# Performance work log

Measured on AMD Instinct MI355X. Metric: run time of the kernel, lower is better.

## Reference

```python
import jax, jax.numpy as jnp
import numpy as np

# DeepSeek-V2-Lite MoE dims
E = 64      # n_routed_experts
H = 2048    # hidden_size
I = 1408    # moe_intermediate_size
K = 6       # num_experts_per_tok (top-k)
T = 1024    # tokens
C = 256     # per-expert capacity (expected load T*K/E = 96; 256 is ample, no drops with seed 0)


def setup_inputs() -> dict:
    key = jax.random.key(0)
    k1, k2, k3, k4 = jax.random.split(key, 4)
    return {
        "hidden_states": jax.random.normal(k1, (T, H), jnp.float32),
        "gate_w": jax.random.normal(k2, (H, E), jnp.float32) * 0.02,   # LiteLinear(H->E), no bias
        "w1": jax.random.normal(k3, (E, H, I), jnp.float32) * 0.02,    # experts_w1
        "w2": jax.random.normal(k4, (E, I, H), jnp.float32) * 0.02,    # experts_w2
    }


def _moe(x, gate_w, w1, w2):
    # Router: softmax gate + top-k + renormalize (vLLM fused_moe renormalize=True)
    logits = x @ gate_w                                    # [T, E]
    probs = jax.nn.softmax(logits, axis=-1)
    topk_w, topk_idx = jax.lax.top_k(probs, K)             # [T, K]
    topk_w = topk_w / jnp.sum(topk_w, axis=-1, keepdims=True)

    # Dispatch: flatten (token, k) pairs, compute slot position within each expert
    P = T * K
    e_p = topk_idx.reshape(P)                              # expert id per pair
    onehot = (e_p[:, None] == jnp.arange(E)[None, :]).astype(jnp.int32)  # [P, E]
    pos = jnp.cumsum(onehot, axis=0) - 1                   # running count per expert
    pos = jnp.take_along_axis(pos, e_p[:, None], axis=1)[:, 0]           # [P]
    valid = pos < C
    pos_c = jnp.where(valid, pos, 0)
    fvalid = valid[:, None].astype(x.dtype)

    x_pair = jnp.repeat(x, K, axis=0)                      # [P, H]
    xe = jnp.zeros((E, C, H), x.dtype).at[e_p, pos_c].add(x_pair * fvalid)  # [E, C, H]

    # Grouped expert GEMMs: silu(x @ w1) @ w2
    h = jax.nn.silu(jnp.einsum('ech,ehi->eci', xe, w1))    # [E, C, I]
    ye = jnp.einsum('eci,eih->ech', h, w2)                 # [E, C, H]

    # Combine: gather back per pair, weight by routing prob, sum over k
    y_pair = ye[e_p, pos_c] * fvalid                       # [P, H]
    out = (y_pair.reshape(T, K, H) * topk_w[..., None]).sum(axis=1)
    return out


def reference(hidden_states, gate_w, w1, w2):
    return _moe(hidden_states, gate_w, w1, w2)
```

## Files before the change

### kernel.cpp

```cpp
#include <hip/hip_runtime.h>

#define T_TOK 1024
#define H_DIM 2048
#define I_DIM 1408
#define E_NUM 64
#define K_TOP 6
#define CAP   256
#define P_NUM (T_TOK * K_TOP)

typedef __bf16 bf16x8 __attribute__((ext_vector_type(8)));
typedef float  f32x4  __attribute__((ext_vector_type(4)));
typedef unsigned int uint32x2 __attribute__((ext_vector_type(2)));
typedef unsigned int uint32x4 __attribute__((ext_vector_type(4)));

__device__ inline unsigned pack2bf16(float a, float b) {
    unsigned short au = __builtin_bit_cast(unsigned short, (__bf16)a);
    unsigned short bu = __builtin_bit_cast(unsigned short, (__bf16)b);
    return (unsigned)au | ((unsigned)bu << 16);
}

__device__ inline void wg_barrier() {
    __builtin_amdgcn_sched_barrier(0);
    asm volatile("s_waitcnt lgkmcnt(0)");
    __builtin_amdgcn_s_barrier();
    __builtin_amdgcn_sched_barrier(0);
}

__global__ __launch_bounds__(256) void router_kernel(
        const float* __restrict__ x, const float* __restrict__ gw,
        float* __restrict__ tw, int* __restrict__ ti, __bf16* __restrict__ xb,
        float* __restrict__ out)
{
    const int t0  = blockIdx.x * 4;
    const int tid = threadIdx.x;
    __shared__ float xs[4][H_DIM];
    __shared__ float part[4][4][E_NUM];

    {
        f32x4 z = (f32x4){0.f, 0.f, 0.f, 0.f};
        f32x4* ob = (f32x4*)(out + (size_t)t0 * H_DIM);
        #pragma unroll
        for (int i = 0; i < 8; ++i) ob[i * 256 + tid] = z;
    }

    #pragma unroll
    for (int tt = 0; tt < 4; ++tt) {
        #pragma unroll
        for (int i = 0; i < 8; ++i) {
            float v = x[(size_t)(t0 + tt) * H_DIM + i * 256 + tid];
            xs[tt][i * 256 + tid] = v;
            xb[(size_t)(t0 + tt) * H_DIM + i * 256 + tid] = (__bf16)v;
        }
    }
    __syncthreads();

    const int e = tid & 63, q = tid >> 6;
    float a0 = 0.f, a1 = 0.f, a2 = 0.f, a3 = 0.f;
    for (int hh = q * 512; hh < q * 512 + 512; ++hh) {
        float g = gw[hh * E_NUM + e];
        a0 += xs[0][hh] * g; a1 += xs[1][hh] * g;
        a2 += xs[2][hh] * g; a3 += xs[3][hh] * g;
    }
    part[q][0][e] = a0; part[q][1][e] = a1; part[q][2][e] = a2; part[q][3][e] = a3;
    __syncthreads();

    const int tt = q;
    float l = part[0][tt][e] + part[1][tt][e] + part[2][tt][e] + part[3][tt][e];
    float m = l;
    #pragma unroll
    for (int s = 32; s; s >>= 1) m = fmaxf(m, __shfl_xor(m, s));
    float p = __expf(l - m);
    float sum = p;
    #pragma unroll
    for (int s = 32; s; s >>= 1) sum += __shfl_xor(sum, s);
    float prob = p / sum;

    float v = prob, wsum = 0.f;
    float tv[K_TOP]; int tix[K_TOP];
    #pragma unroll
    for (int k = 0; k < K_TOP; ++k) {
        float bv = v; int bi = e;
        #pragma unroll
        for (int s = 32; s; s >>= 1) {
            float ov = __shfl_xor(bv, s); int oi = __shfl_xor(bi, s);
            if (ov > bv || (ov == bv && oi < bi)) { bv = ov; bi = oi; }
        }
        tv[k] = bv; tix[k] = bi; wsum += bv;
        if (e == bi) v = -1.0f;
    }
    if (e == 0) {
        #pragma unroll
        for (int k = 0; k < K_TOP; ++k) {
            tw[(t0 + tt) * K_TOP + k] = tv[k] / wsum;
            ti[(t0 + tt) * K_TOP + k] = tix[k];
        }
    }
}

__global__ __launch_bounds__(1024) void dispatch_scan_kernel(
        const int* __restrict__ ti, int* __restrict__ cnt,
        int* __restrict__ base, int* __restrict__ list)
{
    __shared__ int lcnt[E_NUM];
    const int tid = threadIdx.x;
    if (tid < E_NUM) lcnt[tid] = 0;
    __syncthreads();
    #pragma unroll
    for (int i = 0; i < P_NUM / 1024; ++i) {
        int p = i * 1024 + tid;
        int e = ti[p];
        int slot = atomicAdd(&lcnt[e], 1);
        if (slot < CAP) list[e * CAP + slot] = p;
    }
    __syncthreads();
    if (tid == 0) {
        int acc = 0;
        for (int e = 0; e < E_NUM; ++e) {
            base[e] = acc;
            int c = lcnt[e];
            cnt[e] = c;
            if (c > CAP) c = CAP;
            acc += (c + 15) & ~15;
        }
    }
}

#define B_LDB 36

__global__ __launch_bounds__(256, 3) void gemm1_kernel(
        const float* __restrict__ w1, const __bf16* __restrict__ xb,
        const int* __restrict__ cnt, const int* __restrict__ base,
        const int* __restrict__ list, __bf16* __restrict__ hbuf)
{
    const int e  = blockIdx.z;
    const int m0 = blockIdx.y * 128;
    const int nb = blockIdx.x * 128;

    int rows = cnt[e]; if (rows > CAP) rows = CAP;
    const int rows_pad = (rows + 15) & ~15;
    if (m0 >= rows_pad) return;
    int mcount = rows_pad - m0; if (mcount > 128) mcount = 128;
    const int nmf = mcount >> 4;
    const int hb = base[e];

    __shared__ __attribute__((aligned(16))) __bf16 As[128][72];
    __shared__ __attribute__((aligned(16))) unsigned Bs[128 * B_LDB];
    __shared__ int ts[128];

    const int tid = threadIdx.x;
    if (tid < 128) {
        int slot = m0 + tid;
        ts[tid] = (slot < rows) ? (list[e * CAP + slot] / K_TOP) : 0;
    }
    __syncthreads();

    const int lane = tid & 63;
    const int wv   = tid >> 6;
    const int l15  = lane & 15;
    const int lg   = lane >> 4;

    const int sm = tid >> 3;
    const int sk = (tid & 7) << 3;
    const __bf16* ap[4];
    #pragma unroll
    for (int it = 0; it < 4; ++it)
        ap[it] = xb + (size_t)ts[it * 32 + sm] * H_DIM + sk;

    const int c4 = tid & 31;
    const int kb = tid >> 5;
    const int Xw = 4 * ((c4 ^ (c4 >> 3)) & 7);
    const float* bload = w1 + (size_t)e * H_DIM * I_DIM + (nb + 4 * c4);

    int cB0 = wv * 32 + l15;
    int cB1 = cB0 + 16;
    int c4r0 = cB0 >> 2, c4r1 = cB1 >> 2;
    const int Xr0 = 4 * ((c4r0 ^ (c4r0 >> 3)) & 7);
    const int Xr1 = 4 * ((c4r1 ^ (c4r1 >> 3)) & 7);
    const unsigned* bfp0 = Bs + cB0 * B_LDB;
    const unsigned* bfp1 = Bs + cB1 * B_LDB;

    f32x4 acc[8][2];
    #pragma unroll
    for (int m = 0; m < 8; ++m) {
        acc[m][0] = (f32x4){0.f, 0.f, 0.f, 0.f};
        acc[m][1] = (f32x4){0.f, 0.f, 0.f, 0.f};
    }

    f32x4 f[8]; bf16x8 av[4];
    {
        const float* bp = bload;
        #pragma unroll
        for (int r = 0; r < 4; ++r)
            f[r] = __builtin_nontemporal_load((const f32x4*)(bp + (size_t)(4 * kb + r) * I_DIM));
        #pragma unroll
        for (int r = 0; r < 4; ++r)
            f[4 + r] = __builtin_nontemporal_load((const f32x4*)(bp + (size_t)(4 * kb + 32 + r) * I_DIM));
        #pragma unroll
        for (int it = 0; it < 4; ++it) av[it] = *(const bf16x8*)(ap[it]);
    }

    for (int k0 = 0; k0 < H_DIM; k0 += 64) {
        int kn = k0 + 64; if (kn >= H_DIM) kn = 0;
        wg_barrier();
        #pragma unroll
        for (int it = 0; it < 4; ++it)
            *(bf16x8*)(&As[it * 32 + sm][sk]) = av[it];
        #pragma unroll
        for (int b = 0; b < 2; ++b) {
            #pragma unroll
            for (int i = 0; i < 4; ++i) {
                unsigned lo = pack2bf16(f[4 * b + 0][i], f[4 * b + 1][i]);
                unsigned hi = pack2bf16(f[4 * b + 2][i], f[4 * b + 3][i]);
                int c = 4 * c4 + i;
                int p = 2 * kb + 16 * b;
                *(uint32x2*)(&Bs[c * B_LDB + (p ^ Xw)]) = (uint32x2){lo, hi};
            }
        }
        {
            const float* bp = bload + (size_t)(kn + 4 * kb) * I_DIM;
            #pragma unroll
            for (int r = 0; r < 4; ++r)
                f[r] = __builtin_nontemporal_load((const f32x4*)(bp + (size_t)r * I_DIM));
            const float* bp2 = bp + (size_t)32 * I_DIM;
            #pragma unroll
            for (int r = 0; r < 4; ++r)
                f[4 + r] = __builtin_nontemporal_load((const f32x4*)(bp2 + (size_t)r * I_DIM));
            #pragma unroll
            for (int it = 0; it < 4; ++it) av[it] = *(const bf16x8*)(ap[it] + kn);
        }
        wg_barrier();
        #pragma unroll
        for (int ks = 0; ks < 2; ++ks) {
            int pbase = ks * 16 + lg * 4;
            bf16x8 b0 = *(const bf16x8*)(bfp0 + (pbase ^ Xr0));
            bf16x8 b1 = *(const bf16x8*)(bfp1 + (pbase ^ Xr1));
            #pragma unroll
            for (int m = 0; m < 8; ++m) {
                if (m < nmf) {
                    bf16x8 a = *(const bf16x8*)(&As[m * 16 + l15][ks * 32 + lg * 8]);
                    acc[m][0] = __builtin_amdgcn_mfma_f32_16x16x32_bf16(a, b0, acc[m][0], 0, 0, 0);
                    acc[m][1] = __builtin_amdgcn_mfma_f32_16x16x32_bf16(a, b1, acc[m][1], 0, 0, 0);
                }
            }
        }
    }

    const int nw = nb + wv * 32;
    #pragma unroll
    for (int m = 0; m < 8; ++m) {
        if (m < nmf) {
            #pragma unroll
            for (int nf = 0; nf < 2; ++nf) {
                #pragma unroll
                for (int j = 0; j < 4; ++j) {
                    int row = m * 16 + lg * 4 + j;
                    int col = nw + nf * 16 + l15;
                    float v = acc[m][nf][j];
                    float s = v / (1.0f + __expf(-v));
                    hbuf[(size_t)(hb + m0 + row) * I_DIM + col] = (__bf16)s;
                }
            }
        }
    }
}

__global__ __launch_bounds__(256, 2) void gemm2_kernel(
        const float* __restrict__ w2, const __bf16* __restrict__ hbuf,
        const int* __restrict__ cnt, const int* __restrict__ base,
        const int* __restrict__ list, const float* __restrict__ tw,
        float* __restrict__ out)
{
    const int e  = blockIdx.z;
    const int m0 = blockIdx.y * 128;
    const int nb = blockIdx.x * 256;

    int rows = cnt[e]; if (rows > CAP) rows = CAP;
    const int rows_pad = (rows + 15) & ~15;
    if (m0 >= rows_pad) return;
    int mcount = rows_pad - m0; if (mcount > 128) mcount = 128;
    const int nmf = mcount >> 4;
    const int hb = base[e];

    __shared__ __attribute__((aligned(16))) __bf16 As[128][72];
    __shared__ __attribute__((aligned(16))) unsigned Bs[256 * B_LDB];
    __shared__ int ps[128];
    __shared__ float tws[128];

    const int tid = threadIdx.x;
    if (tid < 128) {
        int slot = m0 + tid;
        int p = (slot < rows) ? list[e * CAP + slot] : -1;
        ps[tid] = p;
        tws[tid] = (p >= 0) ? tw[p] : 0.f;
    }
    __syncthreads();

    const int lane = tid & 63;
    const int wv   = tid >> 6;
    const int l15  = lane & 15;
    const int lg   = lane >> 4;
    const int wm   = wv >> 1;
    const int wn   = wv & 1;

    const int sm = tid >> 3;
    const int sk = (tid & 7) << 3;
    const __bf16* abase = hbuf + (size_t)(hb + m0 + sm) * I_DIM + sk;

    const int c4 = tid & 63;
    const int kq = tid >> 6;
    const int Xw = 4 * ((c4 ^ (c4 >> 3)) & 7);
    const float* bload = w2 + (size_t)e * I_DIM * H_DIM
                            + (size_t)(16 * kq) * H_DIM + (nb + 4 * c4);

    f32x4 acc[4][8];
    #pragma unroll
    for (int m = 0; m < 4; ++m)
        #pragma unroll
        for (int nf = 0; nf < 8; ++nf)
            acc[m][nf] = (f32x4){0.f, 0.f, 0.f, 0.f};

    f32x4 f[16]; bf16x8 av[4];
    #pragma unroll
    for (int r = 0; r < 16; ++r)
        f[r] = __builtin_nontemporal_load((const f32x4*)(bload + (size_t)r * H_DIM));
    #pragma unroll
    for (int it = 0; it < 4; ++it)
        av[it] = *(const bf16x8*)(abase + (size_t)(it * 32) * I_DIM);

    for (int k0 = 0; k0 < I_DIM; k0 += 64) {
        int kn = k0 + 64; if (kn >= I_DIM) kn = 0;
        wg_barrier();
        #pragma unroll
        for (int it = 0; it < 4; ++it)
            *(bf16x8*)(&As[it * 32 + sm][sk]) = av[it];
        #pragma unroll
        for (int i = 0; i < 4; ++i) {
            int c = 4 * c4 + i;
            uint32x4 q0, q1;
            #pragma unroll
            for (int r = 0; r < 4; ++r)
                q0[r] = pack2bf16(f[2 * r][i], f[2 * r + 1][i]);
            #pragma unroll
            for (int r = 0; r < 4; ++r)
                q1[r] = pack2bf16(f[8 + 2 * r][i], f[9 + 2 * r][i]);
            *(uint32x4*)(&Bs[c * B_LDB + ((8 * kq) ^ Xw)])     = q0;
            *(uint32x4*)(&Bs[c * B_LDB + ((8 * kq + 4) ^ Xw)]) = q1;
        }
        {
            const float* bp = bload + (size_t)kn * H_DIM;
            #pragma unroll
            for (int r = 0; r < 16; ++r)
                f[r] = __builtin_nontemporal_load((const f32x4*)(bp + (size_t)r * H_DIM));
            #pragma unroll
            for (int it = 0; it < 4; ++it)
                av[it] = *(const bf16x8*)(abase + (size_t)(it * 32) * I_DIM + kn);
        }
        wg_barrier();
        #pragma unroll
        for (int ks = 0; ks < 2; ++ks) {
            int pbase = ks * 16 + lg * 4;
            bf16x8 a[4];
            #pragma unroll
            for (int m = 0; m < 4; ++m)
                a[m] = *(const bf16x8*)(&As[wm * 64 + m * 16 + l15][ks * 32 + lg * 8]);
            #pragma unroll
            for (int nf = 0; nf < 8; ++nf) {
                int col = wn * 128 + nf * 16 + l15;
                int c4r = col >> 2;
                int Xr = 4 * ((c4r ^ (c4r >> 3)) & 7);
                bf16x8 b = *(const bf16x8*)(&Bs[col * B_LDB + (pbase ^ Xr)]);
                #pragma unroll
                for (int m = 0; m < 4; ++m) {
                    if (wm * 4 + m < nmf)
                        acc[m][nf] = __builtin_amdgcn_mfma_f32_16x16x32_bf16(a[m], b, acc[m][nf], 0, 0, 0);
                }
            }
        }
    }

    #pragma unroll
    for (int m = 0; m < 4; ++m) {
        if (wm * 4 + m < nmf) {
            #pragma unroll
            for (int nf = 0; nf < 8; ++nf) {
                #pragma unroll
                for (int j = 0; j < 4; ++j) {
                    int row = wm * 64 + m * 16 + lg * 4 + j;
                    int p = ps[row];
                    if (p >= 0) {
                        int t = p / K_TOP;
                        float v = acc[m][nf][j] * tws[row];
                        atomicAdd(&out[(size_t)t * H_DIM + (nb + wn * 128 + nf * 16 + l15)], v);
                    }
                }
            }
        }
    }
}

extern "C" void kernel_launch(void* const* d_in, const int* in_sizes, int n_in,
                              void* d_out, int out_size, void* d_ws, size_t ws_size,
                              hipStream_t stream) {
    const float* x  = (const float*)d_in[0];
    const float* gw = (const float*)d_in[1];
    const float* w1 = (const float*)d_in[2];
    const float* w2 = (const float*)d_in[3];
    float* out = (float*)d_out;

    char* ws = (char*)d_ws;
    int*    cnt  = (int*)ws;
    int*    base = (int*)(ws + 256);
    int*    list = (int*)(ws + 512);
    float*  tw   = (float*)(ws + 66048);
    int*    ti   = (int*)(ws + 90624);
    __bf16* xb   = (__bf16*)(ws + 131072);
    __bf16* hbuf = (__bf16*)(ws + 4325376);

    hipLaunchKernelGGL(router_kernel, dim3(T_TOK / 4), dim3(256), 0, stream,
                       x, gw, tw, ti, xb, out);
    hipLaunchKernelGGL(dispatch_scan_kernel, dim3(1), dim3(1024), 0, stream,
                       ti, cnt, base, list);
    hipLaunchKernelGGL(gemm1_kernel, dim3(I_DIM / 128, 2, E_NUM), dim3(256), 0, stream,
                       w1, xb, cnt, base, list, hbuf);
    hipLaunchKernelGGL(gemm2_kernel, dim3(H_DIM / 256, 2, E_NUM), dim3(256), 0, stream,
                       w2, hbuf, cnt, base, list, tw, out);
}
```

Measured before the change: 412.3 us.

## Widen gemm1 N-tile to 176 columns with redistributed w1 staging

Changes the gemm1 N-tile from 128 to 176 columns, so I=1408 splits into 8 tiles and the grid shrinks from 11 to 8 column blocks per expert. Each tile of x rows is then reused across more w1 columns, cutting repeated A loads. The w1 load-and-convert path is rewritten so 256 threads move 11 float4 chunks each, with per-element bf16 scalar stores into swizzled LDS. Each wave now handles up to 3 N-fragments, unevenly spread across the 4 waves. Risks are higher register use (occupancy drops to 2 waves per SIMD), scalar LDS stores that may bank-conflict, and wave load imbalance.

```diff
diff --git a/kernel.cpp b/kernel.cpp
--- a/kernel.cpp
+++ b/kernel.cpp
@@ -127,14 +127,14 @@
 
 #define B_LDB 36
 
-__global__ __launch_bounds__(256, 3) void gemm1_kernel(
+__global__ __launch_bounds__(256, 2) void gemm1_kernel(
         const float* __restrict__ w1, const __bf16* __restrict__ xb,
         const int* __restrict__ cnt, const int* __restrict__ base,
         const int* __restrict__ list, __bf16* __restrict__ hbuf)
 {
     const int e  = blockIdx.z;
     const int m0 = blockIdx.y * 128;
-    const int nb = blockIdx.x * 128;
+    const int nb = blockIdx.x * 176;
 
     int rows = cnt[e]; if (rows > CAP) rows = CAP;
     const int rows_pad = (rows + 15) & ~15;
@@ -144,7 +144,7 @@
     const int hb = base[e];
 
     __shared__ __attribute__((aligned(16))) __bf16 As[128][72];
-    __shared__ __attribute__((aligned(16))) unsigned Bs[128 * B_LDB];
+    __shared__ __attribute__((aligned(16))) unsigned Bs[176 * B_LDB];
     __shared__ int ts[128];
 
     const int tid = threadIdx.x;
@@ -166,38 +166,34 @@
     for (int it = 0; it < 4; ++it)
         ap[it] = xb + (size_t)ts[it * 32 + sm] * H_DIM + sk;
 
-    const int c4 = tid & 31;
-    const int kb = tid >> 5;
-    const int Xw = 4 * ((c4 ^ (c4 >> 3)) & 7);
-    const float* bload = w1 + (size_t)e * H_DIM * I_DIM + (nb + 4 * c4);
-
-    int cB0 = wv * 32 + l15;
-    int cB1 = cB0 + 16;
-    int c4r0 = cB0 >> 2, c4r1 = cB1 >> 2;
-    const int Xr0 = 4 * ((c4r0 ^ (c4r0 >> 3)) & 7);
-    const int Xr1 = 4 * ((c4r1 ^ (c4r1 >> 3)) & 7);
-    const unsigned* bfp0 = Bs + cB0 * B_LDB;
-    const unsigned* bfp1 = Bs + cB1 * B_LDB;
-
-    f32x4 acc[8][2];
-    #pragma unroll
-    for (int m = 0; m < 8; ++m) {
-        acc[m][0] = (f32x4){0.f, 0.f, 0.f, 0.f};
-        acc[m][1] = (f32x4){0.f, 0.f, 0.f, 0.f};
-    }
-
-    f32x4 f[8]; bf16x8 av[4];
-    {
-        const float* bp = bload;
-        #pragma unroll
-        for (int r = 0; r < 4; ++r)
-            f[r] = __builtin_nontemporal_load((const f32x4*)(bp + (size_t)(4 * kb + r) * I_DIM));
-        #pragma unroll
-        for (int r = 0; r < 4; ++r)
-            f[4 + r] = __builtin_nontemporal_load((const f32x4*)(bp + (size_t)(4 * kb + 32 + r) * I_DIM));
-        #pragma unroll
-        for (int it = 0; it < 4; ++it) av[it] = *(const bf16x8*)(ap[it]);
-    }
+    const float* bbase = w1 + (size_t)e * H_DIM * I_DIM + nb;
+    int voff[11];
+    int laddr[11];
+    #pragma unroll
+    for (int j = 0; j < 11; ++j) {
+        int u = 256 * j + tid;
+        int kj = u / 44;
+        int c16 = u - 44 * kj;
+        voff[j] = kj * I_DIM + 4 * c16;
+        int Xw = 4 * ((c16 ^ (c16 >> 3)) & 7);
+        int pairb = (kj >> 1) ^ Xw;
+        laddr[j] = (4 * c16 * B_LDB + pairb) * 2 + (kj & 1);
+    }
+    __bf16* bsp = (__bf16*)Bs;
+
+    f32x4 acc[8][3];
+    #pragma unroll
+    for (int m = 0; m < 8; ++m)
+        #pragma unroll
+        for (int nf = 0; nf < 3; ++nf)
+            acc[m][nf] = (f32x4){0.f, 0.f, 0.f, 0.f};
+
+    f32x4 f[11]; bf16x8 av[4];
+    #pragma unroll
+    for (int j = 0; j < 11; ++j)
+        f[j] = __builtin_nontemporal_load((const f32x4*)(bbase + voff[j]));
+    #pragma unroll
+    for (int it = 0; it < 4; ++it) av[it] = *(const bf16x8*)(ap[it]);
 
     for (int k0 = 0; k0 < H_DIM; k0 += 64) {
         int kn = k0 + 64; if (kn >= H_DIM) kn = 0;
@@ -206,25 +202,16 @@
         for (int it = 0; it < 4; ++it)
             *(bf16x8*)(&As[it * 32 + sm][sk]) = av[it];
         #pragma unroll
-        for (int b = 0; b < 2; ++b) {
-            #pragma unroll
-            for (int i = 0; i < 4; ++i) {
-                unsigned lo = pack2bf16(f[4 * b + 0][i], f[4 * b + 1][i]);
-                unsigned hi = pack2bf16(f[4 * b + 2][i], f[4 * b + 3][i]);
-                int c = 4 * c4 + i;
-                int p = 2 * kb + 16 * b;
-                *(uint32x2*)(&Bs[c * B_LDB + (p ^ Xw)]) = (uint32x2){lo, hi};
-            }
+        for (int j = 0; j < 11; ++j) {
+            #pragma unroll
+            for (int i = 0; i < 4; ++i)
+                bsp[laddr[j] + 2 * B_LDB * i] = (__bf16)f[j][i];
         }
         {
-            const float* bp = bload + (size_t)(kn + 4 * kb) * I_DIM;
-            #pragma unroll
-            for (int r = 0; r < 4; ++r)
-                f[r] = __builtin_nontemporal_load((const f32x4*)(bp + (size_t)r * I_DIM));
-            const float* bp2 = bp + (size_t)32 * I_DIM;
-            #pragma unroll
-            for (int r = 0; r < 4; ++r)
-                f[4 + r] = __builtin_nontemporal_load((const f32x4*)(bp2 + (size_t)r * I_DIM));
+            const float* bp = bbase + (size_t)kn * I_DIM;
+            #pragma unroll
+            for (int j = 0; j < 11; ++j)
+                f[j] = __builtin_nontemporal_load((const f32x4*)(bp + voff[j]));
             #pragma unroll
             for (int it = 0; it < 4; ++it) av[it] = *(const bf16x8*)(ap[it] + kn);
         }
@@ -232,32 +219,41 @@
         #pragma unroll
         for (int ks = 0; ks < 2; ++ks) {
             int pbase = ks * 16 + lg * 4;
-            bf16x8 b0 = *(const bf16x8*)(bfp0 + (pbase ^ Xr0));
-            bf16x8 b1 = *(const bf16x8*)(bfp1 + (pbase ^ Xr1));
-            #pragma unroll
-            for (int m = 0; m < 8; ++m) {
-                if (m < nmf) {
-                    bf16x8 a = *(const bf16x8*)(&As[m * 16 + l15][ks * 32 + lg * 8]);
-                    acc[m][0] = __builtin_amdgcn_mfma_f32_16x16x32_bf16(a, b0, acc[m][0], 0, 0, 0);
-                    acc[m][1] = __builtin_amdgcn_mfma_f32_16x16x32_bf16(a, b1, acc[m][1], 0, 0, 0);
+            #pragma unroll
+            for (int nf = 0; nf < 3; ++nf) {
+                int fg = wv + 4 * nf;
+                if (fg < 11) {
+                    int col = 16 * fg + l15;
+                    int c4r = col >> 2;
+                    int Xr = 4 * ((c4r ^ (c4r >> 3)) & 7);
+                    bf16x8 b = *(const bf16x8*)(&Bs[col * B_LDB + (pbase ^ Xr)]);
+                    #pragma unroll
+                    for (int m = 0; m < 8; ++m) {
+                        if (m < nmf) {
+                            bf16x8 a = *(const bf16x8*)(&As[m * 16 + l15][ks * 32 + lg * 8]);
+                            acc[m][nf] = __builtin_amdgcn_mfma_f32_16x16x32_bf16(a, b, acc[m][nf], 0, 0, 0);
+                        }
+                    }
                 }
             }
         }
     }
 
-    const int nw = nb + wv * 32;
     #pragma unroll
     for (int m = 0; m < 8; ++m) {
         if (m < nmf) {
             #pragma unroll
-            for (int nf = 0; nf < 2; ++nf) {
-                #pragma unroll
-                for (int j = 0; j < 4; ++j) {
-                    int row = m * 16 + lg * 4 + j;
-                    int col = nw + nf * 16 + l15;
-                    float v = acc[m][nf][j];
-                    float s = v / (1.0f + __expf(-v));
-                    hbuf[(size_t)(hb + m0 + row) * I_DIM + col] = (__bf16)s;
+            for (int nf = 0; nf < 3; ++nf) {
+                int fg = wv + 4 * nf;
+                if (fg < 11) {
+                    #pragma unroll
+                    for (int j = 0; j < 4; ++j) {
+                        int row = m * 16 + lg * 4 + j;
+                        int col = nb + 16 * fg + l15;
+                        float v = acc[m][nf][j];
+                        float s = v / (1.0f + __expf(-v));
+                        hbuf[(size_t)(hb + m0 + row) * I_DIM + col] = (__bf16)s;
+                    }
                 }
             }
         }
@@ -420,7 +416,7 @@
                        x, gw, tw, ti, xb, out);
     hipLaunchKernelGGL(dispatch_scan_kernel, dim3(1), dim3(1024), 0, stream,
                        ti, cnt, base, list);
-    hipLaunchKernelGGL(gemm1_kernel, dim3(I_DIM / 128, 2, E_NUM), dim3(256), 0, stream,
+    hipLaunchKernelGGL(gemm1_kernel, dim3(I_DIM / 176, 2, E_NUM), dim3(256), 0, stream,
                        w1, xb, cnt, base, list, hbuf);
     hipLaunchKernelGGL(gemm2_kernel, dim3(H_DIM / 256, 2, E_NUM), dim3(256), 0, stream,
                        w2, hbuf, cnt, base, list, tw, out);
```

New measurement: 508.9 us. +23.4%, slower.
